# Optimization experiments

Measured on AMD Instinct MI355X. Metric: run time of the kernel, lower is better.

The kernel has to match this reference:

```python
import jax, jax.numpy as jnp
import numpy as np

B, N, D, HID, H = 2048, 128, 512, 2048, 8
DH = D // H
EPS = 1e-5


def setup_inputs() -> dict:
    key = jax.random.key(0)
    ks = jax.random.split(key, 16)
    s = 0.02
    inp = {
        "catalog_features": jax.random.normal(ks[0], (B, D), jnp.float32),
        "neighbors": jax.random.normal(ks[1], (B, N, D), jnp.float32),
        "lengths": jax.random.randint(ks[2], (B,), 1, N + 1, jnp.int32),
        # FFN params (stored [in, out])
        "W1": jax.random.normal(ks[3], (D, HID), jnp.float32) * s,
        "b1": jnp.zeros((HID,), jnp.float32),
        "gamma": jnp.ones((HID,), jnp.float32),
        "beta": jnp.zeros((HID,), jnp.float32),
        "W2": jax.random.normal(ks[4], (HID, HID), jnp.float32) * s,
        "b2": jnp.zeros((HID,), jnp.float32),
        "W3": jax.random.normal(ks[5], (HID, D), jnp.float32) * s,
        "b3": jnp.zeros((D,), jnp.float32),
        # MultiheadAttention params
        "Wq": jax.random.normal(ks[6], (D, D), jnp.float32) * s,
        "bq": jnp.zeros((D,), jnp.float32),
        "Wk": jax.random.normal(ks[7], (D, D), jnp.float32) * s,
        "bk": jnp.zeros((D,), jnp.float32),
        "Wv": jax.random.normal(ks[8], (D, D), jnp.float32) * s,
        "bv": jnp.zeros((D,), jnp.float32),
        "Wo": jax.random.normal(ks[9], (D, D), jnp.float32) * s,
        "bo": jnp.zeros((D,), jnp.float32),
    }
    return inp


def _ffn(x, W1, b1, gamma, beta, W2, b2, W3, b3):
    x = jnp.tanh(x @ W1 + b1)
    # BatchNorm1d (training-mode batch stats, biased variance, eps=1e-5)
    mu = jnp.mean(x, axis=0)
    var = jnp.mean(jnp.square(x - mu), axis=0)
    x = (x - mu) * jax.lax.rsqrt(var + EPS) * gamma + beta
    x = jnp.tanh(x @ W2 + b2)
    return x @ W3 + b3


def reference(catalog_features, neighbors, lengths, W1, b1, gamma, beta,
              W2, b2, W3, b3, Wq, bq, Wk, bk, Wv, bv, Wo, bo):
    emb = _ffn(catalog_features, W1, b1, gamma, beta, W2, b2, W3, b3)  # [B, D]
    # batched single-query multi-head attention over padded neighbor sets
    q = (emb @ Wq + bq).reshape(B, H, DH)                 # [B, H, DH]
    k = (neighbors @ Wk + bk).reshape(B, N, H, DH)        # [B, N, H, DH]
    v = (neighbors @ Wv + bv).reshape(B, N, H, DH)
    scores = jnp.einsum("bhd,bnhd->bhn", q, k) / np.sqrt(DH).astype(np.float32)
    valid = (jnp.arange(N)[None, :] < lengths[:, None])   # [B, N]
    scores = jnp.where(valid[:, None, :], scores, -jnp.inf)
    attn = jax.nn.softmax(scores, axis=-1)                # [B, H, N]
    ctx = jnp.einsum("bhn,bnhd->bhd", attn, v).reshape(B, D)
    return ctx @ Wo + bo                                   # [B, D]
```

## Files before the change

### kernel.cpp

```cpp
#include <hip/hip_runtime.h>
#include <stdint.h>


typedef unsigned short u16;
typedef unsigned int u32;
typedef __attribute__((ext_vector_type(8))) short bf16x8;
typedef __attribute__((ext_vector_type(4))) float f32x4;

__device__ __forceinline__ float b2f(u16 h){
  union { u32 u; float f; } c; c.u = ((u32)h) << 16; return c.f;
}
__device__ __forceinline__ u16 f2b(float f){
  union { float f; u32 u; } c; c.f = f;
  u32 r = (c.u + 0x7fffu + ((c.u >> 16) & 1u)) >> 16;
  return (u16)r;
}
__device__ __forceinline__ float fast_tanh(float x){
  float ax = fabsf(x);
  float e  = __expf(2.0f * ax);
  float t  = 1.0f - 2.0f / (e + 1.0f);
  return x < 0.0f ? -t : t;
}
__device__ __forceinline__ void gl_lds16(const u16* g, u16* l){
  __builtin_amdgcn_global_load_lds((const __attribute__((address_space(1))) void*)g,
                                   (__attribute__((address_space(3))) void*)l,
                                   16, 0, 0);
}
__device__ __forceinline__ bool isf32(const int* flg){ return *flg > 32; }

__global__ void detect_kernel(const u16* w, int* flag){
  __shared__ int cnt[256];
  int c = 0;
  #pragma unroll
  for (int i = 0; i < 16; ++i){
    u16 v = w[threadIdx.x * 16 + i];
    if (((v >> 7) & 0xff) >= 0xC0) c++;
  }
  cnt[threadIdx.x] = c;
  __syncthreads();
  if (threadIdx.x == 0){
    int s = 0;
    for (int i = 0; i < 256; ++i) s += cnt[i];
    *flag = s;
  }
}

__global__ __launch_bounds__(256) void conv_copy(
    const void* __restrict__ src, u16* __restrict__ dst, int n4, const int* flg)
{
  int i = blockIdx.x * 256 + threadIdx.x;
  if (i >= n4) return;
  if (isf32(flg)){
    float4 v = ((const float4*)src)[i];
    ushort4 o; o.x = f2b(v.x); o.y = f2b(v.y); o.z = f2b(v.z); o.w = f2b(v.w);
    ((ushort4*)dst)[i] = o;
  } else {
    ((ushort4*)dst)[i] = ((const ushort4*)src)[i];
  }
}

__global__ __launch_bounds__(256) void conv_transpose(
    const void* __restrict__ in, u16* __restrict__ out, int R, int Cc, const int* flg)
{
  __shared__ u16 t[32][33];
  int c0 = blockIdx.x * 32, r0 = blockIdx.y * 32;
  int lr = threadIdx.x >> 5, lc = threadIdx.x & 31;
  bool f = isf32(flg);
  #pragma unroll
  for (int p = 0; p < 4; ++p){
    int r = p * 8 + lr;
    size_t idx = (size_t)(r0 + r) * Cc + c0 + lc;
    t[r][lc] = f ? f2b(((const float*)in)[idx]) : ((const u16*)in)[idx];
  }
  __syncthreads();
  #pragma unroll
  for (int p = 0; p < 4; ++p){
    int c = p * 8 + lr;
    out[(size_t)(c0 + c) * R + r0 + lc] = t[lc][c];
  }
}

template<int NT>
__global__ __launch_bounds__(256) void gemm_bt(
    const u16* __restrict__ A, int lda,
    const u16* __restrict__ Bt, int ldb,
    u16* __restrict__ C, int ldc,
    const u16* __restrict__ bias,
    int K, int epi,
    int aOffZ, int bOffZ, int cOffZ, int biasOffZ,
    const int* outflg)
{
  constexpr int BN2 = NT * 16;
  __shared__ u16 As[128 * 32];
  __shared__ u16 Bs[NT * 32 * 32];
  const int z = blockIdx.z;
  A  += (size_t)z * aOffZ;
  Bt += (size_t)z * bOffZ;
  C  += (size_t)z * cOffZ;
  if (bias) bias += z * biasOffZ;

  const int tid = threadIdx.x;
  const int w = tid >> 6, l = tid & 63;
  const int wm = w & 1, wn = w >> 1;
  const int m0 = blockIdx.x * 128;
  const int n0 = blockIdx.y * (NT * 32);
  const int l15 = l & 15;
  const int kq  = (l >> 4) * 8;

  f32x4 acc[4][NT];
  #pragma unroll
  for (int i = 0; i < 4; ++i)
    #pragma unroll
    for (int j = 0; j < NT; ++j)
      acc[i][j] = (f32x4){0.f, 0.f, 0.f, 0.f};

  const int nkt = K >> 5;
  for (int kt = 0; kt < nkt; ++kt){
    const int k0 = kt << 5;
    __syncthreads();
    #pragma unroll
    for (int it = 0; it < 2; ++it){
      int e = (it * 4 + w) * 512 + l * 8;
      gl_lds16(A + (size_t)(m0 + (e >> 5)) * lda + k0 + (e & 31), &As[e]);
    }
    #pragma unroll
    for (int it = 0; it < NT / 2; ++it){
      int e = (it * 4 + w) * 512 + l * 8;
      gl_lds16(Bt + (size_t)(n0 + (e >> 5)) * ldb + k0 + (e & 31), &Bs[e]);
    }
    __syncthreads();
    bf16x8 af[4], bfr[NT];
    #pragma unroll
    for (int mt = 0; mt < 4; ++mt)
      af[mt] = *(const bf16x8*)&As[(wm * 64 + mt * 16 + l15) * 32 + kq];
    #pragma unroll
    for (int nt = 0; nt < NT; ++nt)
      bfr[nt] = *(const bf16x8*)&Bs[(wn * BN2 + nt * 16 + l15) * 32 + kq];
    #pragma unroll
    for (int mt = 0; mt < 4; ++mt)
      #pragma unroll
      for (int nt = 0; nt < NT; ++nt)
        acc[mt][nt] = __builtin_amdgcn_mfma_f32_16x16x32_bf16(af[mt], bfr[nt], acc[mt][nt], 0, 0, 0);
  }

  const bool f32o = outflg && isf32(outflg);
  const int q4 = (l >> 4) * 4;
  #pragma unroll
  for (int nt = 0; nt < NT; ++nt){
    int n = n0 + wn * BN2 + nt * 16 + l15;
    float bb = bias ? b2f(bias[n]) : 0.0f;
    #pragma unroll
    for (int mt = 0; mt < 4; ++mt){
      #pragma unroll
      for (int r = 0; r < 4; ++r){
        int m = m0 + wm * 64 + mt * 16 + q4 + r;
        float x = acc[mt][nt][r] + bb;
        if (epi == 1) x = fast_tanh(x);
        else if (epi == 2) x *= 0.125f;
        if (f32o) ((float*)C)[(size_t)m * ldc + n] = x;
        else      C[(size_t)m * ldc + n] = f2b(x);
      }
    }
  }
}

__global__ __launch_bounds__(256) void bn_stats(
    const u16* __restrict__ X, float* __restrict__ s1, float* __restrict__ s2)
{
  int c  = blockIdx.x * 256 + threadIdx.x;
  int r0 = blockIdx.y * 256;
  float a = 0.f, b = 0.f;
  for (int r = 0; r < 256; ++r){
    float x = b2f(X[(size_t)(r0 + r) * 2048 + c]);
    a += x; b += x * x;
  }
  atomicAdd(&s1[c], a);
  atomicAdd(&s2[c], b);
}

__global__ __launch_bounds__(256) void bn_fin(
    const float* __restrict__ s1, const float* __restrict__ s2,
    const u16* __restrict__ gamma, const u16* __restrict__ beta,
    float* __restrict__ A, float* __restrict__ Cc)
{
  int j = blockIdx.x * 256 + threadIdx.x;
  float mu  = s1[j] * (1.0f / 2048.0f);
  float var = s2[j] * (1.0f / 2048.0f) - mu * mu;
  float a = b2f(gamma[j]) * rsqrtf(var + 1e-5f);
  A[j]  = a;
  Cc[j] = b2f(beta[j]) - mu * a;
}

__global__ __launch_bounds__(256) void bn_apply(
    u16* __restrict__ X, const float* __restrict__ A, const float* __restrict__ Cc)
{
  int i = blockIdx.x * 256 + threadIdx.x;
  uint4 v = ((const uint4*)X)[i];
  u16* p = (u16*)&v;
  int base = i * 8;
  #pragma unroll
  for (int e = 0; e < 8; ++e){
    int j = (base + e) & 2047;
    p[e] = f2b(A[j] * b2f(p[e]) + Cc[j]);
  }
  ((uint4*)X)[i] = v;
}

__global__ __launch_bounds__(256) void att_scores(
    const void* __restrict__ nb_g, const int* __restrict__ lengths,
    const u16* __restrict__ qt_g, u16* __restrict__ attn_g, const int* flg)
{
  __shared__ u16 qtS[16 * 264];
  __shared__ u16 nbS[64 * 264];
  __shared__ float scS[128 * 17];
  const int b = blockIdx.x, tid = threadIdx.x;
  const int w = tid >> 6, l = tid & 63;
  const int l15 = l & 15, kq = (l >> 4) * 8;
  const bool f = isf32(flg);

  for (int n0c = 0; n0c < 2; ++n0c){
    f32x4 acc = (f32x4){0.f, 0.f, 0.f, 0.f};
    for (int dh = 0; dh < 2; ++dh){
      __syncthreads();
      {
        int row = tid >> 5, col8 = (tid & 31) * 8;
        *(uint4*)&qtS[row * 264 + col8] =
            *(const uint4*)&qt_g[(size_t)b * 4096 + row * 512 + dh * 256 + col8];
        uint4 zz; zz.x = zz.y = zz.z = zz.w = 0u;
        *(uint4*)&qtS[(8 + row) * 264 + col8] = zz;
      }
      #pragma unroll
      for (int it = 0; it < 8; ++it){
        int c = it * 256 + tid, row = c >> 5, col8 = (c & 31) * 8;
        size_t base = (size_t)b * 65536 + (size_t)(n0c * 64 + row) * 512 + dh * 256 + col8;
        uint4 v;
        if (f){
          float4 a  = *(const float4*)((const float*)nb_g + base);
          float4 bb = *(const float4*)((const float*)nb_g + base + 4);
          u16* p = (u16*)&v;
          p[0]=f2b(a.x); p[1]=f2b(a.y); p[2]=f2b(a.z); p[3]=f2b(a.w);
          p[4]=f2b(bb.x);p[5]=f2b(bb.y);p[6]=f2b(bb.z);p[7]=f2b(bb.w);
        } else {
          v = *(const uint4*)((const u16*)nb_g + base);
        }
        *(uint4*)&nbS[row * 264 + col8] = v;
      }
      __syncthreads();
      const int n = w * 16 + l15;
      #pragma unroll
      for (int ks = 0; ks < 8; ++ks){
        bf16x8 a  = *(const bf16x8*)&nbS[n * 264 + ks * 32 + kq];
        bf16x8 q8 = *(const bf16x8*)&qtS[l15 * 264 + ks * 32 + kq];
        acc = __builtin_amdgcn_mfma_f32_16x16x32_bf16(a, q8, acc, 0, 0, 0);
      }
    }
    const int q4 = (l >> 4) * 4;
    #pragma unroll
    for (int r = 0; r < 4; ++r)
      scS[(n0c * 64 + w * 16 + q4 + r) * 17 + l15] = acc[r];
  }
  __syncthreads();

  const int len = lengths[b];
  #pragma unroll
  for (int hp = 0; hp < 2; ++hp){
    int h = w + hp * 4;
    float s0 = scS[l * 17 + h], s1 = scS[(64 + l) * 17 + h];
    float m0 = (l < len)      ? s0 : -3.0e38f;
    float m1 = (64 + l < len) ? s1 : -3.0e38f;
    float m = fmaxf(m0, m1);
    #pragma unroll
    for (int o = 32; o > 0; o >>= 1) m = fmaxf(m, __shfl_xor(m, o, 64));
    float e0 = (l < len)      ? __expf(s0 - m) : 0.0f;
    float e1 = (64 + l < len) ? __expf(s1 - m) : 0.0f;
    float s = e0 + e1;
    #pragma unroll
    for (int o = 32; o > 0; o >>= 1) s += __shfl_xor(s, o, 64);
    float inv = 1.0f / s;
    attn_g[(size_t)b * 1024 + h * 128 + l]      = f2b(e0 * inv);
    attn_g[(size_t)b * 1024 + h * 128 + 64 + l] = f2b(e1 * inv);
  }
}

__global__ __launch_bounds__(256) void att_pv(
    const void* __restrict__ nb_g, const u16* __restrict__ attn_g,
    u16* __restrict__ ctxr_g, const int* flg)
{
  __shared__ float atF[1024];
  __shared__ u16 nbS[32 * 512];
  const int b = blockIdx.x, tid = threadIdx.x;
  const bool f = isf32(flg);
  #pragma unroll
  for (int it = 0; it < 4; ++it){
    int i = it * 256 + tid;
    atF[i] = b2f(attn_g[(size_t)b * 1024 + i]);
  }
  float acc[16];
  #pragma unroll
  for (int i = 0; i < 16; ++i) acc[i] = 0.f;

  for (int n0 = 0; n0 < 128; n0 += 32){
    __syncthreads();
    #pragma unroll
    for (int it = 0; it < 8; ++it){
      int c = it * 256 + tid, row = c >> 6, col8 = (c & 63) * 8;
      size_t base = (size_t)b * 65536 + (size_t)(n0 + row) * 512 + col8;
      uint4 v;
      if (f){
        float4 a  = *(const float4*)((const float*)nb_g + base);
        float4 bb = *(const float4*)((const float*)nb_g + base + 4);
        u16* p = (u16*)&v;
        p[0]=f2b(a.x); p[1]=f2b(a.y); p[2]=f2b(a.z); p[3]=f2b(a.w);
        p[4]=f2b(bb.x);p[5]=f2b(bb.y);p[6]=f2b(bb.z);p[7]=f2b(bb.w);
      } else {
        v = *(const uint4*)((const u16*)nb_g + base);
      }
      *(uint4*)&nbS[row * 512 + col8] = v;
    }
    __syncthreads();
    #pragma unroll 4
    for (int n = 0; n < 32; ++n){
      float v0 = b2f(nbS[n * 512 + tid]);
      float v1 = b2f(nbS[n * 512 + 256 + tid]);
      #pragma unroll
      for (int h = 0; h < 8; ++h){
        float a = atF[h * 128 + n0 + n];
        acc[h]     += a * v0;
        acc[8 + h] += a * v1;
      }
    }
  }
  #pragma unroll
  for (int h = 0; h < 8; ++h){
    ctxr_g[(size_t)b * 4096 + h * 512 + tid]       = f2b(acc[h]);
    ctxr_g[(size_t)b * 4096 + h * 512 + 256 + tid] = f2b(acc[8 + h]);
  }
}

extern "C" void kernel_launch(void* const* d_in, const int* in_sizes, int n_in,
                              void* d_out, int out_size, void* d_ws, size_t ws_size,
                              hipStream_t stream)
{
  (void)in_sizes; (void)n_in; (void)out_size; (void)ws_size;
  const void* cat   = d_in[0];
  const void* nbg   = d_in[1];
  const int*  len   = (const int*)d_in[2];
  const void* W1    = d_in[3];
  const void* b1    = d_in[4];
  const void* gamma = d_in[5];
  const void* beta  = d_in[6];
  const void* W2    = d_in[7];
  const void* b2    = d_in[8];
  const void* W3    = d_in[9];
  const void* b3    = d_in[10];
  const void* Wq    = d_in[11];
  const void* bq    = d_in[12];
  const void* Wk    = d_in[13];
  const void* Wv    = d_in[15];
  const void* bv    = d_in[16];
  const void* Wo    = d_in[17];
  const void* bo    = d_in[18];

  char* ws = (char*)d_ws;
  u16* X1   = (u16*)(ws + 0);
  u16* X2   = (u16*)(ws + 8388608);
  u16* qt   = (u16*)(ws + 0);
  u16* ctxr = qt;
  u16* emb  = (u16*)(ws + 16777216);
  u16* q    = (u16*)(ws + 18874368);
  u16* ctx  = (u16*)(ws + 20971520);
  u16* attn = (u16*)(ws + 23068672);
  u16* catB = (u16*)(ws + 27262976);
  u16* WkB  = (u16*)(ws + 29360128);
  u16* W1T  = (u16*)(ws + 29884416);
  u16* W2T  = (u16*)(ws + 31981568);
  u16* W3T  = (u16*)(ws + 40370176);
  u16* WqT  = (u16*)(ws + 42467328);
  u16* WvT  = (u16*)(ws + 42991616);
  u16* WoT  = (u16*)(ws + 43515904);
  u16* bB   = (u16*)(ws + 44040192);
  float* s1 = (float*)(ws + 44060672);
  float* s2 = (float*)(ws + 44068864);
  float* bnA= (float*)(ws + 44077056);
  float* bnC= (float*)(ws + 44085248);
  int* flag = (int*)(ws + 44093440);

  u16 *b1B = bB, *gmB = bB + 2048, *btB = bB + 4096, *b2B = bB + 6144;
  u16 *b3B = bB + 8192, *bqB = bB + 8704, *bvB = bB + 9216, *boB = bB + 9728;

  detect_kernel<<<1, 256, 0, stream>>>((const u16*)W1, flag);

  conv_copy<<<1024, 256, 0, stream>>>(cat, catB, 262144, flag);
  conv_copy<<<256, 256, 0, stream>>>(Wk, WkB, 65536, flag);
  conv_copy<<<2, 256, 0, stream>>>(b1, b1B, 512, flag);
  conv_copy<<<2, 256, 0, stream>>>(gamma, gmB, 512, flag);
  conv_copy<<<2, 256, 0, stream>>>(beta, btB, 512, flag);
  conv_copy<<<2, 256, 0, stream>>>(b2, b2B, 512, flag);
  conv_copy<<<1, 256, 0, stream>>>(b3, b3B, 128, flag);
  conv_copy<<<1, 256, 0, stream>>>(bq, bqB, 128, flag);
  conv_copy<<<1, 256, 0, stream>>>(bv, bvB, 128, flag);
  conv_copy<<<1, 256, 0, stream>>>(bo, boB, 128, flag);

  conv_transpose<<<dim3(64, 16), 256, 0, stream>>>(W1, W1T, 512, 2048, flag);
  conv_transpose<<<dim3(64, 64), 256, 0, stream>>>(W2, W2T, 2048, 2048, flag);
  conv_transpose<<<dim3(16, 64), 256, 0, stream>>>(W3, W3T, 2048, 512, flag);
  conv_transpose<<<dim3(16, 16), 256, 0, stream>>>(Wq, WqT, 512, 512, flag);
  conv_transpose<<<dim3(16, 16), 256, 0, stream>>>(Wv, WvT, 512, 512, flag);
  conv_transpose<<<dim3(16, 16), 256, 0, stream>>>(Wo, WoT, 512, 512, flag);

  hipMemsetAsync(s1, 0, 16384, stream);

  gemm_bt<4><<<dim3(16, 16), 256, 0, stream>>>(catB, 512, W1T, 512, X1, 2048, b1B, 512, 1, 0, 0, 0, 0, nullptr);
  bn_stats<<<dim3(8, 8), 256, 0, stream>>>(X1, s1, s2);
  bn_fin  <<<8, 256, 0, stream>>>(s1, s2, gmB, btB, bnA, bnC);
  bn_apply<<<2048, 256, 0, stream>>>(X1, bnA, bnC);
  gemm_bt<4><<<dim3(16, 16), 256, 0, stream>>>(X1, 2048, W2T, 2048, X2, 2048, b2B, 2048, 1, 0, 0, 0, 0, nullptr);
  gemm_bt<4><<<dim3(16, 4), 256, 0, stream>>>(X2, 2048, W3T, 2048, emb, 512, b3B, 2048, 0, 0, 0, 0, 0, nullptr);

  gemm_bt<4><<<dim3(16, 4), 256, 0, stream>>>(emb, 512, WqT, 512, q, 512, bqB, 512, 2, 0, 0, 0, 0, nullptr);
  gemm_bt<4><<<dim3(16, 4, 8), 256, 0, stream>>>(q, 512, WkB, 512, qt, 4096, nullptr, 64, 0, 64, 64, 512, 0, nullptr);

  att_scores<<<2048, 256, 0, stream>>>(nbg, len, qt, attn, flag);
  att_pv<<<2048, 256, 0, stream>>>(nbg, attn, ctxr, flag);

  gemm_bt<2><<<dim3(16, 1, 8), 256, 0, stream>>>(ctxr, 4096, WvT, 512, ctx, 512, bvB, 512, 0, 512, 32768, 64, 64, nullptr);

  gemm_bt<4><<<dim3(16, 4), 256, 0, stream>>>(ctx, 512, WoT, 512, (u16*)d_out, 512, boB, 512, 0, 0, 0, 0, 0, flag);
}
```

Before: 1.092 ms.

## Fuse attention score and PV kernels, batch conversion launches

```diff
diff --git a/kernel.cpp b/kernel.cpp
--- a/kernel.cpp
+++ b/kernel.cpp
@@ -45,25 +45,57 @@
   }
 }
 
-__global__ __launch_bounds__(256) void conv_copy(
-    const void* __restrict__ src, u16* __restrict__ dst, int n4, const int* flg)
-{
-  int i = blockIdx.x * 256 + threadIdx.x;
-  if (i >= n4) return;
+struct CopyArgs {
+  const void* src[10];
+  u16* dst[10];
+  int end[10];
+};
+
+__global__ __launch_bounds__(256) void conv_copy_multi(
+    CopyArgs a, int total, const int* __restrict__ flg)
+{
+  int g = blockIdx.x * 256 + threadIdx.x;
+  if (g >= total) return;
+  const void* sp = a.src[0]; u16* dp = a.dst[0]; int base = 0;
+  #pragma unroll
+  for (int k = 1; k < 10; ++k){
+    if (g >= a.end[k-1]){ sp = a.src[k]; dp = a.dst[k]; base = a.end[k-1]; }
+  }
+  int i = g - base;
   if (isf32(flg)){
-    float4 v = ((const float4*)src)[i];
+    float4 v = ((const float4*)sp)[i];
     ushort4 o; o.x = f2b(v.x); o.y = f2b(v.y); o.z = f2b(v.z); o.w = f2b(v.w);
-    ((ushort4*)dst)[i] = o;
+    ((ushort4*)dp)[i] = o;
   } else {
-    ((ushort4*)dst)[i] = ((const ushort4*)src)[i];
-  }
-}
-
-__global__ __launch_bounds__(256) void conv_transpose(
-    const void* __restrict__ in, u16* __restrict__ out, int R, int Cc, const int* flg)
+    ((ushort4*)dp)[i] = ((const ushort4*)sp)[i];
+  }
+}
+
+struct TpArgs {
+  const void* src[6];
+  u16* dst[6];
+  int R[6];
+  int C[6];
+  int tX[6];
+  int start[6];
+};
+
+__global__ __launch_bounds__(256) void conv_transpose_multi(
+    TpArgs a, const int* __restrict__ flg)
 {
   __shared__ u16 t[32][33];
-  int c0 = blockIdx.x * 32, r0 = blockIdx.y * 32;
+  const int bid = blockIdx.x;
+  const void* in = a.src[0]; u16* out = a.dst[0];
+  int R = a.R[0], Cc = a.C[0], tX = a.tX[0], base = 0;
+  #pragma unroll
+  for (int k = 1; k < 6; ++k){
+    if (bid >= a.start[k]){
+      in = a.src[k]; out = a.dst[k];
+      R = a.R[k]; Cc = a.C[k]; tX = a.tX[k]; base = a.start[k];
+    }
+  }
+  int lid = bid - base;
+  int c0 = (lid % tX) * 32, r0 = (lid / tX) * 32;
   int lr = threadIdx.x >> 5, lc = threadIdx.x & 31;
   bool f = isf32(flg);
   #pragma unroll
@@ -206,66 +238,67 @@
   ((uint4*)X)[i] = v;
 }
 
-__global__ __launch_bounds__(256) void att_scores(
+__global__ __launch_bounds__(512) void att_fused(
     const void* __restrict__ nb_g, const int* __restrict__ lengths,
-    const u16* __restrict__ qt_g, u16* __restrict__ attn_g, const int* flg)
-{
-  __shared__ u16 qtS[16 * 264];
-  __shared__ u16 nbS[64 * 264];
-  __shared__ float scS[128 * 17];
+    const u16* __restrict__ qt_g, u16* __restrict__ ctxr_g, const int* flg)
+{
+  __shared__ u16 nbS[128 * 520];
+  __shared__ u16 qtS[16 * 520];
+  __shared__ float scS[128 * 9];
+  __shared__ float atT[128 * 8];
   const int b = blockIdx.x, tid = threadIdx.x;
   const int w = tid >> 6, l = tid & 63;
   const int l15 = l & 15, kq = (l >> 4) * 8;
   const bool f = isf32(flg);
 
-  for (int n0c = 0; n0c < 2; ++n0c){
+  {
+    int i = tid * 8;
+    int row = i >> 9, col = i & 511;
+    *(uint4*)&qtS[row * 520 + col] = *(const uint4*)&qt_g[(size_t)b * 4096 + i];
+    uint4 zz; zz.x = zz.y = zz.z = zz.w = 0u;
+    *(uint4*)&qtS[(8 + row) * 520 + col] = zz;
+  }
+  #pragma unroll
+  for (int it = 0; it < 16; ++it){
+    int c = (it * 512 + tid) * 8;
+    int row = c >> 9, col = c & 511;
+    size_t base = (size_t)b * 65536 + c;
+    uint4 v;
+    if (f){
+      float4 a  = *(const float4*)((const float*)nb_g + base);
+      float4 bb = *(const float4*)((const float*)nb_g + base + 4);
+      u16* p = (u16*)&v;
+      p[0]=f2b(a.x); p[1]=f2b(a.y); p[2]=f2b(a.z); p[3]=f2b(a.w);
+      p[4]=f2b(bb.x);p[5]=f2b(bb.y);p[6]=f2b(bb.z);p[7]=f2b(bb.w);
+    } else {
+      v = *(const uint4*)((const u16*)nb_g + base);
+    }
+    *(uint4*)&nbS[row * 520 + col] = v;
+  }
+  __syncthreads();
+
+  {
     f32x4 acc = (f32x4){0.f, 0.f, 0.f, 0.f};
-    for (int dh = 0; dh < 2; ++dh){
-      __syncthreads();
-      {
-        int row = tid >> 5, col8 = (tid & 31) * 8;
-        *(uint4*)&qtS[row * 264 + col8] =
-            *(const uint4*)&qt_g[(size_t)b * 4096 + row * 512 + dh * 256 + col8];
-        uint4 zz; zz.x = zz.y = zz.z = zz.w = 0u;
-        *(uint4*)&qtS[(8 + row) * 264 + col8] = zz;
-      }
+    const int n = w * 16 + l15;
+    #pragma unroll
+    for (int ks = 0; ks < 16; ++ks){
+      bf16x8 a  = *(const bf16x8*)&nbS[n * 520 + ks * 32 + kq];
+      bf16x8 q8 = *(const bf16x8*)&qtS[l15 * 520 + ks * 32 + kq];
+      acc = __builtin_amdgcn_mfma_f32_16x16x32_bf16(a, q8, acc, 0, 0, 0);
+    }
+    const int q4 = (l >> 4) * 4;
+    if (l15 < 8){
       #pragma unroll
-      for (int it = 0; it < 8; ++it){
-        int c = it * 256 + tid, row = c >> 5, col8 = (c & 31) * 8;
-        size_t base = (size_t)b * 65536 + (size_t)(n0c * 64 + row) * 512 + dh * 256 + col8;
-        uint4 v;
-        if (f){
-          float4 a  = *(const float4*)((const float*)nb_g + base);
-          float4 bb = *(const float4*)((const float*)nb_g + base + 4);
-          u16* p = (u16*)&v;
-          p[0]=f2b(a.x); p[1]=f2b(a.y); p[2]=f2b(a.z); p[3]=f2b(a.w);
-          p[4]=f2b(bb.x);p[5]=f2b(bb.y);p[6]=f2b(bb.z);p[7]=f2b(bb.w);
-        } else {
-          v = *(const uint4*)((const u16*)nb_g + base);
-        }
-        *(uint4*)&nbS[row * 264 + col8] = v;
-      }
-      __syncthreads();
-      const int n = w * 16 + l15;
-      #pragma unroll
-      for (int ks = 0; ks < 8; ++ks){
-        bf16x8 a  = *(const bf16x8*)&nbS[n * 264 + ks * 32 + kq];
-        bf16x8 q8 = *(const bf16x8*)&qtS[l15 * 264 + ks * 32 + kq];
-        acc = __builtin_amdgcn_mfma_f32_16x16x32_bf16(a, q8, acc, 0, 0, 0);
-      }
-    }
-    const int q4 = (l >> 4) * 4;
-    #pragma unroll
-    for (int r = 0; r < 4; ++r)
-      scS[(n0c * 64 + w * 16 + q4 + r) * 17 + l15] = acc[r];
+      for (int r = 0; r < 4; ++r)
+        scS[(w * 16 + q4 + r) * 9 + l15] = acc[r];
+    }
   }
   __syncthreads();
 
-  const int len = lengths[b];
-  #pragma unroll
-  for (int hp = 0; hp < 2; ++hp){
-    int h = w + hp * 4;
-    float s0 = scS[l * 17 + h], s1 = scS[(64 + l) * 17 + h];
+  {
+    const int len = lengths[b];
+    const int h = w;
+    float s0 = scS[l * 9 + h], s1 = scS[(64 + l) * 9 + h];
     float m0 = (l < len)      ? s0 : -3.0e38f;
     float m1 = (64 + l < len) ? s1 : -3.0e38f;
     float m = fmaxf(m0, m1);
@@ -277,63 +310,37 @@
     #pragma unroll
     for (int o = 32; o > 0; o >>= 1) s += __shfl_xor(s, o, 64);
     float inv = 1.0f / s;
-    attn_g[(size_t)b * 1024 + h * 128 + l]      = f2b(e0 * inv);
-    attn_g[(size_t)b * 1024 + h * 128 + 64 + l] = f2b(e1 * inv);
-  }
-}
-
-__global__ __launch_bounds__(256) void att_pv(
-    const void* __restrict__ nb_g, const u16* __restrict__ attn_g,
-    u16* __restrict__ ctxr_g, const int* flg)
-{
-  __shared__ float atF[1024];
-  __shared__ u16 nbS[32 * 512];
-  const int b = blockIdx.x, tid = threadIdx.x;
-  const bool f = isf32(flg);
-  #pragma unroll
-  for (int it = 0; it < 4; ++it){
-    int i = it * 256 + tid;
-    atF[i] = b2f(attn_g[(size_t)b * 1024 + i]);
-  }
-  float acc[16];
-  #pragma unroll
-  for (int i = 0; i < 16; ++i) acc[i] = 0.f;
-
-  for (int n0 = 0; n0 < 128; n0 += 32){
-    __syncthreads();
-    #pragma unroll
-    for (int it = 0; it < 8; ++it){
-      int c = it * 256 + tid, row = c >> 6, col8 = (c & 63) * 8;
-      size_t base = (size_t)b * 65536 + (size_t)(n0 + row) * 512 + col8;
-      uint4 v;
-      if (f){
-        float4 a  = *(const float4*)((const float*)nb_g + base);
-        float4 bb = *(const float4*)((const float*)nb_g + base + 4);
-        u16* p = (u16*)&v;
-        p[0]=f2b(a.x); p[1]=f2b(a.y); p[2]=f2b(a.z); p[3]=f2b(a.w);
-        p[4]=f2b(bb.x);p[5]=f2b(bb.y);p[6]=f2b(bb.z);p[7]=f2b(bb.w);
-      } else {
-        v = *(const uint4*)((const u16*)nb_g + base);
-      }
-      *(uint4*)&nbS[row * 512 + col8] = v;
-    }
-    __syncthreads();
+    atT[l * 8 + h]        = e0 * inv;
+    atT[(64 + l) * 8 + h] = e1 * inv;
+  }
+  __syncthreads();
+
+  if (tid < 256){
+    float a0[8], a1[8];
+    #pragma unroll
+    for (int h = 0; h < 8; ++h){ a0[h] = 0.f; a1[h] = 0.f; }
     #pragma unroll 4
-    for (int n = 0; n < 32; ++n){
-      float v0 = b2f(nbS[n * 512 + tid]);
-      float v1 = b2f(nbS[n * 512 + 256 + tid]);
-      #pragma unroll
-      for (int h = 0; h < 8; ++h){
-        float a = atF[h * 128 + n0 + n];
-        acc[h]     += a * v0;
-        acc[8 + h] += a * v1;
-      }
-    }
-  }
-  #pragma unroll
-  for (int h = 0; h < 8; ++h){
-    ctxr_g[(size_t)b * 4096 + h * 512 + tid]       = f2b(acc[h]);
-    ctxr_g[(size_t)b * 4096 + h * 512 + 256 + tid] = f2b(acc[8 + h]);
+    for (int n = 0; n < 128; ++n){
+      u32 vv = *(const u32*)&nbS[n * 520 + tid * 2];
+      union { u32 u; float f; } c0, c1;
+      c0.u = vv << 16;
+      c1.u = vv & 0xffff0000u;
+      float4 p0 = *(const float4*)&atT[n * 8];
+      float4 p1 = *(const float4*)&atT[n * 8 + 4];
+      a0[0] += p0.x * c0.f; a1[0] += p0.x * c1.f;
+      a0[1] += p0.y * c0.f; a1[1] += p0.y * c1.f;
+      a0[2] += p0.z * c0.f; a1[2] += p0.z * c1.f;
+      a0[3] += p0.w * c0.f; a1[3] += p0.w * c1.f;
+      a0[4] += p1.x * c0.f; a1[4] += p1.x * c1.f;
+      a0[5] += p1.y * c0.f; a1[5] += p1.y * c1.f;
+      a0[6] += p1.z * c0.f; a1[6] += p1.z * c1.f;
+      a0[7] += p1.w * c0.f; a1[7] += p1.w * c1.f;
+    }
+    #pragma unroll
+    for (int h = 0; h < 8; ++h){
+      u32 o = (u32)f2b(a0[h]) | ((u32)f2b(a1[h]) << 16);
+      ((u32*)ctxr_g)[(size_t)b * 2048 + h * 256 + tid] = o;
+    }
   }
 }
 
@@ -369,7 +376,6 @@
   u16* emb  = (u16*)(ws + 16777216);
   u16* q    = (u16*)(ws + 18874368);
   u16* ctx  = (u16*)(ws + 20971520);
-  u16* attn = (u16*)(ws + 23068672);
   u16* catB = (u16*)(ws + 27262976);
   u16* WkB  = (u16*)(ws + 29360128);
   u16* W1T  = (u16*)(ws + 29884416);
@@ -390,23 +396,34 @@
 
   detect_kernel<<<1, 256, 0, stream>>>((const u16*)W1, flag);
 
-  conv_copy<<<1024, 256, 0, stream>>>(cat, catB, 262144, flag);
-  conv_copy<<<256, 256, 0, stream>>>(Wk, WkB, 65536, flag);
-  conv_copy<<<2, 256, 0, stream>>>(b1, b1B, 512, flag);
-  conv_copy<<<2, 256, 0, stream>>>(gamma, gmB, 512, flag);
-  conv_copy<<<2, 256, 0, stream>>>(beta, btB, 512, flag);
-  conv_copy<<<2, 256, 0, stream>>>(b2, b2B, 512, flag);
-  conv_copy<<<1, 256, 0, stream>>>(b3, b3B, 128, flag);
-  conv_copy<<<1, 256, 0, stream>>>(bq, bqB, 128, flag);
-  conv_copy<<<1, 256, 0, stream>>>(bv, bvB, 128, flag);
-  conv_copy<<<1, 256, 0, stream>>>(bo, boB, 128, flag);
-
-  conv_transpose<<<dim3(64, 16), 256, 0, stream>>>(W1, W1T, 512, 2048, flag);
-  conv_transpose<<<dim3(64, 64), 256, 0, stream>>>(W2, W2T, 2048, 2048, flag);
-  conv_transpose<<<dim3(16, 64), 256, 0, stream>>>(W3, W3T, 2048, 512, flag);
-  conv_transpose<<<dim3(16, 16), 256, 0, stream>>>(Wq, WqT, 512, 512, flag);
-  conv_transpose<<<dim3(16, 16), 256, 0, stream>>>(Wv, WvT, 512, 512, flag);
-  conv_transpose<<<dim3(16, 16), 256, 0, stream>>>(Wo, WoT, 512, 512, flag);
+  {
+    CopyArgs ca;
+    const void* csrc[10] = {cat, Wk, b1, gamma, beta, b2, b3, bq, bv, bo};
+    u16* cdst[10] = {catB, WkB, b1B, gmB, btB, b2B, b3B, bqB, bvB, boB};
+    const int cnt[10] = {262144, 65536, 512, 512, 512, 512, 128, 128, 128, 128};
+    int acc = 0;
+    for (int i = 0; i < 10; ++i){
+      ca.src[i] = csrc[i]; ca.dst[i] = cdst[i];
+      acc += cnt[i]; ca.end[i] = acc;
+    }
+    conv_copy_multi<<<(acc + 255) / 256, 256, 0, stream>>>(ca, acc, flag);
+  }
+
+  {
+    TpArgs ta;
+    const void* tsrc[6] = {W1, W2, W3, Wq, Wv, Wo};
+    u16* tdst[6] = {W1T, W2T, W3T, WqT, WvT, WoT};
+    const int tR[6] = {512, 2048, 2048, 512, 512, 512};
+    const int tC[6] = {2048, 2048, 512, 512, 512, 512};
+    int s = 0;
+    for (int i = 0; i < 6; ++i){
+      ta.src[i] = tsrc[i]; ta.dst[i] = tdst[i];
+      ta.R[i] = tR[i]; ta.C[i] = tC[i]; ta.tX[i] = tC[i] / 32;
+      ta.start[i] = s;
+      s += (tC[i] / 32) * (tR[i] / 32);
+    }
+    conv_transpose_multi<<<s, 256, 0, stream>>>(ta, flag);
+  }
 
   hipMemsetAsync(s1, 0, 16384, stream);
 
@@ -420,8 +437,7 @@
   gemm_bt<4><<<dim3(16, 4), 256, 0, stream>>>(emb, 512, WqT, 512, q, 512, bqB, 512, 2, 0, 0, 0, 0, nullptr);
   gemm_bt<4><<<dim3(16, 4, 8), 256, 0, stream>>>(q, 512, WkB, 512, qt, 4096, nullptr, 64, 0, 64, 64, 512, 0, nullptr);
 
-  att_scores<<<2048, 256, 0, stream>>>(nbg, len, qt, attn, flag);
-  att_pv<<<2048, 256, 0, stream>>>(nbg, attn, ctxr, flag);
+  att_fused<<<2048, 512, 0, stream>>>(nbg, len, qt, ctxr, flag);
 
   gemm_bt<2><<<dim3(16, 1, 8), 256, 0, stream>>>(ctxr, 4096, WvT, 512, ctx, 512, bvB, 512, 0, 512, 32768, 64, 64, nullptr);
 
```

Measured after the change: 1.024 ms. -6.2%, faster.
